# Optimization experiments

Measured on AMD Instinct MI355X. Metric: run time of the kernel, lower is better.

The kernel has to match this reference:

```python
import jax, jax.numpy as jnp
import numpy as np

E = 8        # num_experts
D = 512      # embed_size
H = 8        # attention heads
HD = D // H  # head dim
B, S = 4, 1024


def setup_inputs() -> dict:
    key = jax.random.key(0)
    ks = jax.random.split(key, 16)
    sd = 0.02
    return {
        "x":  jax.random.normal(ks[0], (B, S, D), jnp.float32),
        # per-expert FFN params, stacked over expert dim
        "W1": jax.random.normal(ks[1], (E, D, 4 * D), jnp.float32) * sd,
        "b1": jnp.zeros((E, 4 * D), jnp.float32),
        "W2": jax.random.normal(ks[2], (E, 4 * D, D), jnp.float32) * sd,
        "b2": jnp.zeros((E, D), jnp.float32),
        # MultiheadAttention in_proj (split) and out_proj
        "Wq": jax.random.normal(ks[3], (D, D), jnp.float32) * sd,
        "bq": jnp.zeros((D,), jnp.float32),
        "Wk": jax.random.normal(ks[4], (D, D), jnp.float32) * sd,
        "bk": jnp.zeros((D,), jnp.float32),
        "Wv": jax.random.normal(ks[5], (D, D), jnp.float32) * sd,
        "bv": jnp.zeros((D,), jnp.float32),
        "Wo": jax.random.normal(ks[6], (D, D), jnp.float32) * sd,
        "bo": jnp.zeros((D,), jnp.float32),
        "expert_id": 3,
    }


def reference(x, W1, b1, W2, b2, Wq, bq, Wk, bk, Wv, bv, Wo, bo, expert_id):
    # --- batched per-expert FFN (fuses the Python loop over experts) ---
    # hidden: [B, E, S, 4D]
    hidden = jax.nn.relu(jnp.einsum('bsd,edf->besf', x, W1) + b1[None, :, None, :])
    eo = jnp.einsum('besf,efd->besd', hidden, W2) + b2[None, :, None, :]  # [B,E,S,D]
    eo = eo.transpose(0, 2, 1, 3)  # [B, S, E, D]

    Bs, Ss = x.shape[0], x.shape[1]
    a = eo.reshape(Bs * Ss, E, D)  # [N, E, D]; attention runs over the expert dim

    # --- MultiheadAttention (batch_first), torch semantics ---
    # NOTE: the original passes a FLOAT tril-of-ones attn_mask, which torch ADDS
    # to the scores (it does NOT mask with -inf). We reproduce that faithfully.
    q = (a @ Wq.T + bq).reshape(-1, E, H, HD).transpose(0, 2, 1, 3)  # [N,H,E,hd]
    k = (a @ Wk.T + bk).reshape(-1, E, H, HD).transpose(0, 2, 1, 3)
    v = (a @ Wv.T + bv).reshape(-1, E, H, HD).transpose(0, 2, 1, 3)

    mask = jnp.tril(jnp.ones((E, E), jnp.float32))  # additive float mask
    scores = jnp.einsum('nhed,nhfd->nhef', q, k) / jnp.sqrt(jnp.float32(HD))
    scores = scores + mask[None, None, :, :]
    attn = jax.nn.softmax(scores, axis=-1)
    ctx = jnp.einsum('nhef,nhfd->nhed', attn, v)           # [N,H,E,hd]
    ctx = ctx.transpose(0, 2, 1, 3).reshape(-1, E, D)       # [N,E,D]
    out = ctx @ Wo.T + bo                                   # [N,E,D]

    out = out.reshape(Bs, Ss, E, D)
    return out[:, :, expert_id, :]  # [B, S, D]
```

## Files before the change

### kernel.cpp

```cpp
#include <hip/hip_runtime.h>
#include <hip/hip_bf16.h>

typedef __hip_bfloat16 bf16;
typedef __attribute__((ext_vector_type(4))) float f32x4;
typedef __attribute__((ext_vector_type(8))) short s16x8;

#define N_TOK 4096
#define Dm    512
#define Fm    2048
#define Em    8

__device__ __forceinline__ float bf2f(bf16 v) { return __bfloat162float(v); }
__device__ __forceinline__ bf16  f2bf(float f) { return __float2bfloat16(f); }

#define GL16(g, l)                                                              \
  __builtin_amdgcn_global_load_lds(                                             \
      (const __attribute__((address_space(1))) void*)(g),                       \
      (__attribute__((address_space(3))) void*)(l), 16, 0, 0)

#define BAR()                                   \
  do {                                          \
    __builtin_amdgcn_s_barrier();               \
    asm volatile("" ::: "memory");              \
  } while (0)

__global__ void cvt_f32_bf16(const float* __restrict__ in, bf16* __restrict__ out, int n4) {
  int i = blockIdx.x * 256 + threadIdx.x;
  if (i >= n4) return;
  float4 v = reinterpret_cast<const float4*>(in)[i];
  bf16 tmp[4] = {f2bf(v.x), f2bf(v.y), f2bf(v.z), f2bf(v.w)};
  __builtin_memcpy(out + (size_t)i * 4, tmp, 8);
}

__global__ void cvt_weights(const float* __restrict__ Wq, const float* __restrict__ Wk,
                            const float* __restrict__ Wv, const float* __restrict__ Wo,
                            const float* __restrict__ bk, const float* __restrict__ bv,
                            bf16* __restrict__ qw, bf16* __restrict__ kvw,
                            bf16* __restrict__ ow, float* __restrict__ bkv) {
  int b = blockIdx.x;
  if (b < 1024) {
    int which = b >> 8;
    int i = (b & 255) * 256 + threadIdx.x;
    const float* src = which == 0 ? Wq : which == 1 ? Wk : which == 2 ? Wv : Wo;
    bf16* dst = which == 0 ? qw : which == 1 ? kvw
              : which == 2 ? (kvw + (size_t)Dm * Dm) : ow;
    float4 v = reinterpret_cast<const float4*>(src)[i];
    bf16 tmp[4] = {f2bf(v.x), f2bf(v.y), f2bf(v.z), f2bf(v.w)};
    __builtin_memcpy(dst + (size_t)i * 4, tmp, 8);
  } else {
    for (int j = threadIdx.x; j < Dm; j += 256) {
      bkv[j] = bk[j];
      bkv[Dm + j] = bv[j];
    }
  }
}

__global__ void transpose_cvt(const float* __restrict__ in, bf16* __restrict__ out,
                              int R, int C, long inb, long outb) {
  in  += (long)blockIdx.z * inb;
  out += (long)blockIdx.z * outb;
  __shared__ float t[32][33];
  int tx = threadIdx.x & 31, ty = threadIdx.x >> 5;
  int c0 = blockIdx.x * 32, r0 = blockIdx.y * 32;
#pragma unroll
  for (int i = 0; i < 32; i += 8)
    t[ty + i][tx] = in[(long)(r0 + ty + i) * C + c0 + tx];
  __syncthreads();
#pragma unroll
  for (int i = 0; i < 32; i += 8)
    out[(long)(c0 + ty + i) * R + r0 + tx] = f2bf(t[tx][ty + i]);
}

template <bool RELU, bool OUT_BF16>
__global__ __launch_bounds__(256, 4) void gemm128d(
    const bf16* __restrict__ A, const bf16* __restrict__ Bt, void* __restrict__ Cout,
    const float* __restrict__ bias, int K, int lda, int ldb, int ldc,
    long abs_, long bbs, long cbs, long biasbs,
    const int* __restrict__ eid, int eid_scale) {
  __shared__ bf16 As[2][128 * 32];
  __shared__ bf16 Bs[2][128 * 32];

  int e = blockIdx.z;
  A    += (long)e * abs_;
  Bt   += (long)e * bbs;
  bias += (long)e * biasbs;
  long coff = (long)e * cbs;
  if (eid) A += (long)(*eid) * eid_scale;

  int bm = blockIdx.x * 128, bn = blockIdx.y * 128;
  int tid = threadIdx.x, wv = tid >> 6, lane = tid & 63;
  int wm = wv >> 1, wn = wv & 1;
  int la = lane & 15, q = lane >> 4;
  int srow = lane >> 2;

  const bf16* Ab = A + (long)bm * lda;
  const bf16* Bb = Bt + (long)bn * ldb;
  int nt = K >> 5;

  auto stage = [&](int t) {
    if (t >= nt) return;
    int k0 = t << 5;
    bf16* abuf = &As[t & 1][0];
    bf16* bbuf = &Bs[t & 1][0];
#pragma unroll
    for (int i = 0; i < 2; ++i) {
      int r = wv * 32 + i * 16 + srow;
      int c = (lane & 3) ^ ((r >> 1) & 3);
      GL16(Ab + (long)r * lda + k0 + c * 8, abuf + (wv * 32 + i * 16) * 32);
      GL16(Bb + (long)r * ldb + k0 + c * 8, bbuf + (wv * 32 + i * 16) * 32);
    }
  };

  f32x4 acc[4][4] = {};

  stage(0);

  for (int t = 0; t < nt; ++t) {
    asm volatile("s_waitcnt vmcnt(0)" ::: "memory");
    BAR();
    stage(t + 1);
    const bf16* Abuf = &As[t & 1][0];
    const bf16* Bbuf = &Bs[t & 1][0];
    s16x8 af[4], bfr[4];
#pragma unroll
    for (int m = 0; m < 4; ++m) {
      int r = wm * 64 + m * 16 + la;
      af[m] = *reinterpret_cast<const s16x8*>(Abuf + r * 32 + (q ^ ((r >> 1) & 3)) * 8);
    }
#pragma unroll
    for (int n = 0; n < 4; ++n) {
      int r = wn * 64 + n * 16 + la;
      bfr[n] = *reinterpret_cast<const s16x8*>(Bbuf + r * 32 + (q ^ ((r >> 1) & 3)) * 8);
    }
    __builtin_amdgcn_s_setprio(1);
#pragma unroll
    for (int m = 0; m < 4; ++m)
#pragma unroll
      for (int n = 0; n < 4; ++n)
        acc[m][n] = __builtin_amdgcn_mfma_f32_16x16x32_bf16(bfr[n], af[m], acc[m][n], 0, 0, 0);
    __builtin_amdgcn_s_setprio(0);
  }

#pragma unroll
  for (int m = 0; m < 4; ++m) {
    int gm = bm + wm * 64 + m * 16 + la;
#pragma unroll
    for (int n = 0; n < 4; ++n) {
      int gn = bn + wn * 64 + n * 16 + q * 4;
      float4 b4 = *reinterpret_cast<const float4*>(bias + gn);
      float v0 = acc[m][n][0] + b4.x, v1 = acc[m][n][1] + b4.y;
      float v2 = acc[m][n][2] + b4.z, v3 = acc[m][n][3] + b4.w;
      if (RELU) {
        v0 = fmaxf(v0, 0.f); v1 = fmaxf(v1, 0.f);
        v2 = fmaxf(v2, 0.f); v3 = fmaxf(v3, 0.f);
      }
      long idx = coff + (long)gm * ldc + gn;
      if (OUT_BF16) {
        bf16 tmp[4] = {f2bf(v0), f2bf(v1), f2bf(v2), f2bf(v3)};
        __builtin_memcpy((bf16*)Cout + idx, tmp, 8);
      } else {
        float tmp[4] = {v0, v1, v2, v3};
        __builtin_memcpy((float*)Cout + idx, tmp, 16);
      }
    }
  }
}

__global__ __launch_bounds__(256) void attn_kernel(const float* __restrict__ q,
                                                   const bf16* __restrict__ kv,
                                                   bf16* __restrict__ ctx,
                                                   const int* __restrict__ eid) {
  int wave = threadIdx.x >> 6, lane = threadIdx.x & 63;
  int n = blockIdx.x * 4 + wave;
  int h = lane >> 3, f = lane & 7;
  int e3 = *eid;
  const bf16* kvn = kv + (long)n * Em * (2 * Dm);
  const float* qh = q + (long)n * Dm + h * 64;
  const bf16* kf = kvn + f * (2 * Dm) + h * 64;
  float s = 0.f;
#pragma unroll
  for (int j = 0; j < 64; j++) s += qh[j] * bf2f(kf[j]);
  s *= 0.125f;
  s += (f <= e3) ? 1.0f : 0.0f;
  float mx = s;
#pragma unroll
  for (int d = 1; d < 8; d <<= 1) mx = fmaxf(mx, __shfl_xor(mx, d));
  float ex = expf(s - mx);
  float sm = ex;
#pragma unroll
  for (int d = 1; d < 8; d <<= 1) sm += __shfl_xor(sm, d);
  float at = ex / sm;
  int g = f;
  float acc[8] = {0, 0, 0, 0, 0, 0, 0, 0};
#pragma unroll
  for (int f2 = 0; f2 < 8; f2++) {
    float a = __shfl(at, (h << 3) | f2);
    const bf16* vf = kvn + f2 * (2 * Dm) + Dm + h * 64 + g * 8;
#pragma unroll
    for (int j = 0; j < 8; j++) acc[j] += a * bf2f(vf[j]);
  }
  bf16 tmp[8];
#pragma unroll
  for (int j = 0; j < 8; j++) tmp[j] = f2bf(acc[j]);
  __builtin_memcpy(ctx + (long)n * Dm + h * 64 + g * 8, tmp, 16);
}

extern "C" void kernel_launch(void* const* d_in, const int* in_sizes, int n_in,
                              void* d_out, int out_size, void* d_ws, size_t ws_size,
                              hipStream_t stream) {
  const float* x  = (const float*)d_in[0];
  const float* W1 = (const float*)d_in[1];
  const float* b1 = (const float*)d_in[2];
  const float* W2 = (const float*)d_in[3];
  const float* b2 = (const float*)d_in[4];
  const float* Wq = (const float*)d_in[5];
  const float* bq = (const float*)d_in[6];
  const float* Wk = (const float*)d_in[7];
  const float* bk = (const float*)d_in[8];
  const float* Wv = (const float*)d_in[9];
  const float* bv = (const float*)d_in[10];
  const float* Wo = (const float*)d_in[11];
  const float* bo = (const float*)d_in[12];
  const int* eid  = (const int*)d_in[13];

  char* w = (char*)d_ws;
  auto alloc = [&](size_t bytes) {
    char* p = w;
    w += (bytes + 255) & ~(size_t)255;
    return p;
  };
  bf16* xb   = (bf16*)alloc((size_t)N_TOK * Dm * 2);
  bf16* W1t  = (bf16*)alloc((size_t)Em * Fm * Dm * 2);
  bf16* W2t  = (bf16*)alloc((size_t)Em * Dm * Fm * 2);
  bf16* qw   = (bf16*)alloc((size_t)Dm * Dm * 2);
  bf16* kvw  = (bf16*)alloc((size_t)2 * Dm * Dm * 2);
  bf16* ow   = (bf16*)alloc((size_t)Dm * Dm * 2);
  float* bkv = (float*)alloc((size_t)2 * Dm * 4);
  bf16* hid  = (bf16*)alloc((size_t)Em * N_TOK * Fm * 2);
  bf16* eo   = (bf16*)alloc((size_t)N_TOK * Em * Dm * 2);
  bf16* kv   = (bf16*)hid;
  float* qb  = (float*)(hid + (size_t)N_TOK * Em * 2 * Dm);
  bf16* ctxb = (bf16*)(qb + (size_t)N_TOK * Dm);

  cvt_f32_bf16<<<(N_TOK * Dm / 4 + 255) / 256, 256, 0, stream>>>(x, xb, N_TOK * Dm / 4);
  transpose_cvt<<<dim3(Fm / 32, Dm / 32, Em), 256, 0, stream>>>(
      W1, W1t, Dm, Fm, (long)Dm * Fm, (long)Fm * Dm);
  transpose_cvt<<<dim3(Dm / 32, Fm / 32, Em), 256, 0, stream>>>(
      W2, W2t, Fm, Dm, (long)Fm * Dm, (long)Dm * Fm);
  cvt_weights<<<1025, 256, 0, stream>>>(Wq, Wk, Wv, Wo, bk, bv, qw, kvw, ow, bkv);

  gemm128d<true, true><<<dim3(32, 16, Em), 256, 0, stream>>>(
      xb, W1t, hid, b1, Dm, Dm, Dm, Fm,
      0L, (long)Fm * Dm, (long)N_TOK * Fm, (long)Fm, nullptr, 0);
  gemm128d<false, true><<<dim3(32, 4, Em), 256, 0, stream>>>(
      hid, W2t, eo, b2, Fm, Fm, Fm, Em * Dm,
      (long)N_TOK * Fm, (long)Dm * Fm, (long)Dm, (long)Dm, nullptr, 0);
  gemm128d<false, true><<<dim3(256, 8, 1), 256, 0, stream>>>(
      eo, kvw, kv, bkv, Dm, Dm, Dm, 2 * Dm,
      0L, 0L, 0L, 0L, nullptr, 0);
  gemm128d<false, false><<<dim3(32, 4, 1), 256, 0, stream>>>(
      eo, qw, qb, bq, Dm, Em * Dm, Dm, Dm,
      0L, 0L, 0L, 0L, eid, Dm);
  attn_kernel<<<N_TOK / 4, 256, 0, stream>>>(qb, kv, ctxb, eid);
  gemm128d<false, false><<<dim3(32, 4, 1), 256, 0, stream>>>(
      ctxb, ow, (float*)d_out, bo, Dm, Dm, Dm, Dm,
      0L, 0L, 0L, 0L, nullptr, 0);
}
```

Before: 327.8 us.

## Replace double-buffered K=32 GEMM with single-buffer K=64 tiles; merge conversion kernels

The GEMM drops its double-buffered 32-wide K pipeline, which issued the next stage's global-to-LDS loads before computing the current one. It now loads a single 64-wide K tile per iteration with two __syncthreads and an 8-way XOR swizzle, and also drops the s_setprio hints. The intent is to halve the number of barriers per K element and widen each LDS step, at the cost of losing overlap between memory loads and MFMA work. Separately, the x conversion and the small weight conversions are merged into one launch, and the transpose writes 8-byte packed bf16 stores instead of scalar stores.

```diff
diff --git a/kernel.cpp b/kernel.cpp
--- a/kernel.cpp
+++ b/kernel.cpp
@@ -18,29 +18,22 @@
       (const __attribute__((address_space(1))) void*)(g),                       \
       (__attribute__((address_space(3))) void*)(l), 16, 0, 0)
 
-#define BAR()                                   \
-  do {                                          \
-    __builtin_amdgcn_s_barrier();               \
-    asm volatile("" ::: "memory");              \
-  } while (0)
-
-__global__ void cvt_f32_bf16(const float* __restrict__ in, bf16* __restrict__ out, int n4) {
-  int i = blockIdx.x * 256 + threadIdx.x;
-  if (i >= n4) return;
-  float4 v = reinterpret_cast<const float4*>(in)[i];
-  bf16 tmp[4] = {f2bf(v.x), f2bf(v.y), f2bf(v.z), f2bf(v.w)};
-  __builtin_memcpy(out + (size_t)i * 4, tmp, 8);
-}
-
-__global__ void cvt_weights(const float* __restrict__ Wq, const float* __restrict__ Wk,
-                            const float* __restrict__ Wv, const float* __restrict__ Wo,
-                            const float* __restrict__ bk, const float* __restrict__ bv,
-                            bf16* __restrict__ qw, bf16* __restrict__ kvw,
-                            bf16* __restrict__ ow, float* __restrict__ bkv) {
+__global__ void cvt_all(const float* __restrict__ x, const float* __restrict__ Wq,
+                        const float* __restrict__ Wk, const float* __restrict__ Wv,
+                        const float* __restrict__ Wo, const float* __restrict__ bk,
+                        const float* __restrict__ bv, bf16* __restrict__ xb,
+                        bf16* __restrict__ qw, bf16* __restrict__ kvw,
+                        bf16* __restrict__ ow, float* __restrict__ bkv) {
   int b = blockIdx.x;
-  if (b < 1024) {
-    int which = b >> 8;
-    int i = (b & 255) * 256 + threadIdx.x;
+  if (b < 2048) {
+    int i = b * 256 + threadIdx.x;
+    float4 v = reinterpret_cast<const float4*>(x)[i];
+    bf16 tmp[4] = {f2bf(v.x), f2bf(v.y), f2bf(v.z), f2bf(v.w)};
+    __builtin_memcpy(xb + (size_t)i * 4, tmp, 8);
+  } else if (b < 3072) {
+    int bb = b - 2048;
+    int which = bb >> 8;
+    int i = (bb & 255) * 256 + threadIdx.x;
     const float* src = which == 0 ? Wq : which == 1 ? Wk : which == 2 ? Wv : Wo;
     bf16* dst = which == 0 ? qw : which == 1 ? kvw
               : which == 2 ? (kvw + (size_t)Dm * Dm) : ow;
@@ -60,85 +53,75 @@
   in  += (long)blockIdx.z * inb;
   out += (long)blockIdx.z * outb;
   __shared__ float t[32][33];
-  int tx = threadIdx.x & 31, ty = threadIdx.x >> 5;
+  int tid = threadIdx.x;
+  int col = tid & 31, row8 = tid >> 5;
   int c0 = blockIdx.x * 32, r0 = blockIdx.y * 32;
 #pragma unroll
-  for (int i = 0; i < 32; i += 8)
-    t[ty + i][tx] = in[(long)(r0 + ty + i) * C + c0 + tx];
+  for (int i = 0; i < 4; ++i)
+    t[row8 + i * 8][col] = in[(long)(r0 + row8 + i * 8) * C + c0 + col];
   __syncthreads();
-#pragma unroll
-  for (int i = 0; i < 32; i += 8)
-    out[(long)(c0 + ty + i) * R + r0 + tx] = f2bf(t[tx][ty + i]);
+  int cc = tid >> 3, rb = (tid & 7) * 4;
+  bf16 tmp[4];
+#pragma unroll
+  for (int k = 0; k < 4; ++k) tmp[k] = f2bf(t[rb + k][cc]);
+  __builtin_memcpy(out + (long)(c0 + cc) * R + r0 + rb, tmp, 8);
 }
 
 template <bool RELU, bool OUT_BF16>
-__global__ __launch_bounds__(256, 4) void gemm128d(
+__global__ __launch_bounds__(256, 4) void gemm128(
     const bf16* __restrict__ A, const bf16* __restrict__ Bt, void* __restrict__ Cout,
     const float* __restrict__ bias, int K, int lda, int ldb, int ldc,
     long abs_, long bbs, long cbs, long biasbs,
     const int* __restrict__ eid, int eid_scale) {
-  __shared__ bf16 As[2][128 * 32];
-  __shared__ bf16 Bs[2][128 * 32];
-
-  int e = blockIdx.z;
+  __shared__ bf16 As[128 * 64];
+  __shared__ bf16 Bs[128 * 64];
+
+  int e  = blockIdx.z;
+  int bm = blockIdx.x * 128, bn = blockIdx.y * 128;
+
   A    += (long)e * abs_;
   Bt   += (long)e * bbs;
   bias += (long)e * biasbs;
   long coff = (long)e * cbs;
   if (eid) A += (long)(*eid) * eid_scale;
 
-  int bm = blockIdx.x * 128, bn = blockIdx.y * 128;
   int tid = threadIdx.x, wv = tid >> 6, lane = tid & 63;
   int wm = wv >> 1, wn = wv & 1;
-  int la = lane & 15, q = lane >> 4;
-  int srow = lane >> 2;
 
   const bf16* Ab = A + (long)bm * lda;
   const bf16* Bb = Bt + (long)bn * ldb;
-  int nt = K >> 5;
-
-  auto stage = [&](int t) {
-    if (t >= nt) return;
-    int k0 = t << 5;
-    bf16* abuf = &As[t & 1][0];
-    bf16* bbuf = &Bs[t & 1][0];
-#pragma unroll
-    for (int i = 0; i < 2; ++i) {
-      int r = wv * 32 + i * 16 + srow;
-      int c = (lane & 3) ^ ((r >> 1) & 3);
-      GL16(Ab + (long)r * lda + k0 + c * 8, abuf + (wv * 32 + i * 16) * 32);
-      GL16(Bb + (long)r * ldb + k0 + c * 8, bbuf + (wv * 32 + i * 16) * 32);
-    }
-  };
 
   f32x4 acc[4][4] = {};
-
-  stage(0);
-
-  for (int t = 0; t < nt; ++t) {
-    asm volatile("s_waitcnt vmcnt(0)" ::: "memory");
-    BAR();
-    stage(t + 1);
-    const bf16* Abuf = &As[t & 1][0];
-    const bf16* Bbuf = &Bs[t & 1][0];
-    s16x8 af[4], bfr[4];
-#pragma unroll
-    for (int m = 0; m < 4; ++m) {
-      int r = wm * 64 + m * 16 + la;
-      af[m] = *reinterpret_cast<const s16x8*>(Abuf + r * 32 + (q ^ ((r >> 1) & 3)) * 8);
-    }
-#pragma unroll
-    for (int n = 0; n < 4; ++n) {
-      int r = wn * 64 + n * 16 + la;
-      bfr[n] = *reinterpret_cast<const s16x8*>(Bbuf + r * 32 + (q ^ ((r >> 1) & 3)) * 8);
-    }
-    __builtin_amdgcn_s_setprio(1);
-#pragma unroll
-    for (int m = 0; m < 4; ++m)
+  int la = lane & 15, q = lane >> 4;
+  int srow_lo = lane >> 3;
+
+  for (int k0 = 0; k0 < K; k0 += 64) {
+    __syncthreads();
+#pragma unroll
+    for (int j = 0; j < 4; ++j) {
+      int r = (wv * 4 + j) * 8 + srow_lo;
+      int c = (lane & 7) ^ (r & 7);
+      GL16(Ab + (long)r * lda + k0 + c * 8, As + (wv * 4 + j) * 512);
+      GL16(Bb + (long)r * ldb + k0 + c * 8, Bs + (wv * 4 + j) * 512);
+    }
+    __syncthreads();
+
+#pragma unroll
+    for (int kk = 0; kk < 2; ++kk) {
+      int ps = (kk * 4 + q) ^ (la & 7);
+      s16x8 af[4], bfr[4];
+#pragma unroll
+      for (int m = 0; m < 4; ++m)
+        af[m] = *reinterpret_cast<const s16x8*>(As + (wm * 64 + m * 16 + la) * 64 + ps * 8);
 #pragma unroll
       for (int n = 0; n < 4; ++n)
-        acc[m][n] = __builtin_amdgcn_mfma_f32_16x16x32_bf16(bfr[n], af[m], acc[m][n], 0, 0, 0);
-    __builtin_amdgcn_s_setprio(0);
+        bfr[n] = *reinterpret_cast<const s16x8*>(Bs + (wn * 64 + n * 16 + la) * 64 + ps * 8);
+#pragma unroll
+      for (int m = 0; m < 4; ++m)
+#pragma unroll
+        for (int n = 0; n < 4; ++n)
+          acc[m][n] = __builtin_amdgcn_mfma_f32_16x16x32_bf16(bfr[n], af[m], acc[m][n], 0, 0, 0);
+    }
   }
 
 #pragma unroll
@@ -242,27 +225,26 @@
   float* qb  = (float*)(hid + (size_t)N_TOK * Em * 2 * Dm);
   bf16* ctxb = (bf16*)(qb + (size_t)N_TOK * Dm);
 
-  cvt_f32_bf16<<<(N_TOK * Dm / 4 + 255) / 256, 256, 0, stream>>>(x, xb, N_TOK * Dm / 4);
+  cvt_all<<<3073, 256, 0, stream>>>(x, Wq, Wk, Wv, Wo, bk, bv, xb, qw, kvw, ow, bkv);
   transpose_cvt<<<dim3(Fm / 32, Dm / 32, Em), 256, 0, stream>>>(
       W1, W1t, Dm, Fm, (long)Dm * Fm, (long)Fm * Dm);
   transpose_cvt<<<dim3(Dm / 32, Fm / 32, Em), 256, 0, stream>>>(
       W2, W2t, Fm, Dm, (long)Fm * Dm, (long)Dm * Fm);
-  cvt_weights<<<1025, 256, 0, stream>>>(Wq, Wk, Wv, Wo, bk, bv, qw, kvw, ow, bkv);
-
-  gemm128d<true, true><<<dim3(32, 16, Em), 256, 0, stream>>>(
+
+  gemm128<true, true><<<dim3(32, 16, Em), 256, 0, stream>>>(
       xb, W1t, hid, b1, Dm, Dm, Dm, Fm,
       0L, (long)Fm * Dm, (long)N_TOK * Fm, (long)Fm, nullptr, 0);
-  gemm128d<false, true><<<dim3(32, 4, Em), 256, 0, stream>>>(
+  gemm128<false, true><<<dim3(32, 4, Em), 256, 0, stream>>>(
       hid, W2t, eo, b2, Fm, Fm, Fm, Em * Dm,
       (long)N_TOK * Fm, (long)Dm * Fm, (long)Dm, (long)Dm, nullptr, 0);
-  gemm128d<false, true><<<dim3(256, 8, 1), 256, 0, stream>>>(
+  gemm128<false, true><<<dim3(256, 8, 1), 256, 0, stream>>>(
       eo, kvw, kv, bkv, Dm, Dm, Dm, 2 * Dm,
       0L, 0L, 0L, 0L, nullptr, 0);
-  gemm128d<false, false><<<dim3(32, 4, 1), 256, 0, stream>>>(
+  gemm128<false, false><<<dim3(32, 4, 1), 256, 0, stream>>>(
       eo, qw, qb, bq, Dm, Em * Dm, Dm, Dm,
       0L, 0L, 0L, 0L, eid, Dm);
   attn_kernel<<<N_TOK / 4, 256, 0, stream>>>(qb, kv, ctxb, eid);
-  gemm128d<false, false><<<dim3(32, 4, 1), 256, 0, stream>>>(
+  gemm128<false, false><<<dim3(32, 4, 1), 256, 0, stream>>>(
       ctxb, ow, (float*)d_out, bo, Dm, Dm, Dm, Dm,
       0L, 0L, 0L, 0L, nullptr, 0);
 }
```

Result: faster. 296.0 us (-9.7%).
